# Optimization experiments

Measured on AMD Instinct MI355X. Metric: run time of the kernel, lower is better.

Reference implementation:

```python
import jax, jax.numpy as jnp
import numpy as np

TOKEN_SELF_ATTN_VALUE = -5e4  # reformer_pytorch constant for masking self-attention
BUCKET_SIZE = 64
N_HASHES = 4
HEADS = 8


def look_one_back(x):
    # concat each chunk with the previous chunk along the within-chunk axis (axis=2)
    prev = jnp.concatenate([x[:, -1:], x[:, :-1]], axis=1)
    return jnp.concatenate([prev, x], axis=2)


def lsh_attention(qk, v, rotations):
    # qk, v: (b*h, t, dh); rotations: (dh, n_hashes, n_buckets//2)
    bh, seqlen, dim = qk.shape
    n_buckets = seqlen // BUCKET_SIZE
    # --- LSH bucket hashing via random rotations ---
    rotated = jnp.einsum('btf,fhi->bhti', qk, rotations)            # (bh, H, t, nb/2)
    rotated = jnp.concatenate([rotated, -rotated], axis=-1)          # (bh, H, t, nb)
    buckets = jnp.argmax(rotated, axis=-1)                           # (bh, H, t)
    offsets = (jnp.arange(N_HASHES) * n_buckets)[None, :, None]
    buckets = (buckets + offsets).reshape(bh, N_HASHES * seqlen)
    # --- stable sort tokens by (bucket, position) ---
    ticker = jnp.arange(N_HASHES * seqlen)
    buckets_and_t = seqlen * buckets + (ticker % seqlen)[None, :]
    sticker = jnp.argsort(buckets_and_t, axis=-1)                    # sorted ticker
    undo_sort = jnp.argsort(sticker, axis=-1)
    st = sticker % seqlen                                            # original positions
    sqk = jnp.take_along_axis(qk, st[..., None], axis=1)
    sv = jnp.take_along_axis(v, st[..., None], axis=1)
    # --- chunk into n_hashes*n_buckets chunks of bucket_size tokens ---
    n_chunks = N_HASHES * n_buckets
    bq_t = st.reshape(bh, n_chunks, -1)
    bqk = sqk.reshape(bh, n_chunks, -1, dim)
    bv = sv.reshape(bh, n_chunks, -1, dim)
    bq = bqk
    bk = bqk / jnp.maximum(jnp.linalg.norm(bqk, axis=-1, keepdims=True), 1e-12)
    bk = look_one_back(bk)
    bv = look_one_back(bv)
    bkv_t = look_one_back(bq_t)
    # --- chunked attention with one-chunk lookback ---
    dots = jnp.einsum('bcie,bcje->bcij', bq, bk) * (dim ** -0.5)     # (bh, nc, bs, 2*bs)
    dots = jnp.where(bq_t[:, :, :, None] == bkv_t[:, :, None, :], TOKEN_SELF_ATTN_VALUE, dots)
    dots_lse = jax.nn.logsumexp(dots, axis=-1, keepdims=True)
    probs = jnp.exp(dots - dots_lse)
    bo = jnp.einsum('bcij,bcje->bcie', probs, bv)
    so = bo.reshape(bh, N_HASHES * seqlen, dim)
    slogits = dots_lse.reshape(bh, N_HASHES * seqlen)
    # --- unsort and combine hash rounds weighted by logsumexp ---
    o = jnp.take_along_axis(so, undo_sort[..., None], axis=1)
    logits = jnp.take_along_axis(slogits, undo_sort, axis=1)
    o = o.reshape(bh, N_HASHES, seqlen, dim)
    logits = logits.reshape(bh, N_HASHES, seqlen, 1)
    w = jnp.exp(logits - jax.nn.logsumexp(logits, axis=1, keepdims=True))
    return jnp.sum(o * w, axis=1)


def _forward(queries, Wqk, Wv, Wo, bo, rotations):
    B, N, C = queries.shape
    m = BUCKET_SIZE * 2
    if N % m != 0:  # fit_length: zero-pad to multiple of bucket_size*2 (static)
        pad = m - N % m
        x = jnp.concatenate([queries, jnp.zeros((B, pad, C), queries.dtype)], axis=1)
    else:
        x = queries
    T = x.shape[1]
    dh = C // HEADS
    qk = jnp.einsum('btc,cf->btf', x, Wqk).reshape(B, T, HEADS, dh).transpose(0, 2, 1, 3).reshape(B * HEADS, T, dh)
    v = jnp.einsum('btc,cf->btf', x, Wv).reshape(B, T, HEADS, dh).transpose(0, 2, 1, 3).reshape(B * HEADS, T, dh)
    out = lsh_attention(qk, v, rotations)
    out = out.reshape(B, HEADS, T, dh).transpose(0, 2, 1, 3).reshape(B, T, C)
    out = jnp.einsum('btc,cf->btf', out, Wo) + bo
    return out[:, :N]


def setup_inputs() -> dict:
    key = jax.random.key(0)
    ks = jax.random.split(key, 7)
    B, N, C = 4, 4096, 512
    dh = C // HEADS
    n_buckets = N // BUCKET_SIZE  # 64
    return {
        'queries': jax.random.normal(ks[0], (B, N, C), jnp.float32),
        'keys': jax.random.normal(ks[1], (B, N, C), jnp.float32),
        'values': jax.random.normal(ks[2], (B, N, C), jnp.float32),
        'attn_mask': jnp.zeros((1,), jnp.bool_),
        'tau': 1,
        'delta': 1,
        'Wqk': jax.random.normal(ks[3], (C, C), jnp.float32) / np.float32(np.sqrt(C)),
        'Wv': jax.random.normal(ks[4], (C, C), jnp.float32) / np.float32(np.sqrt(C)),
        'Wo': jax.random.normal(ks[5], (C, C), jnp.float32) / np.float32(np.sqrt(C)),
        'bo': jnp.zeros((C,), jnp.float32),
        'rotations': jax.random.normal(ks[6], (dh, N_HASHES, n_buckets // 2), jnp.float32),
    }


def reference(queries, keys, values, attn_mask, tau, delta, Wqk, Wv, Wo, bo, rotations):
    # keys/values/attn_mask/tau/delta are accepted but unused, matching the torch module
    return _forward(queries, Wqk, Wv, Wo, bo, rotations)
```

## Files before the change

kernel.cpp:

```cpp
#include <hip/hip_runtime.h>
#include <hip/hip_bf16.h>
#include <cstdint>
#include <cstddef>

#define LSEQ   4096
#define DHD    64
#define NHASH  4
#define CDIM   512
#define NBH    32
#define MROWS  16384
#define NCHUNK 256

typedef __attribute__((ext_vector_type(8))) short short8;
typedef __attribute__((ext_vector_type(4))) float f32x4;
typedef __attribute__((ext_vector_type(2))) float f32x2;

__device__ inline uint32_t f2bf(float f) {
  uint32_t u = __float_as_uint(f);
  return (u + 0x7FFFu + ((u >> 16) & 1u)) >> 16;
}
__device__ inline float bf2f(uint32_t h) { return __uint_as_float(h << 16); }
__device__ inline void split2(float f, uint32_t& hi, uint32_t& lo) {
  hi = f2bf(f);
  lo = f2bf(f - bf2f(hi));
}
__device__ inline short8 ldsK(const uint16_t* p) {
  union { uint2 u[2]; short8 s; } t;
  t.u[0] = *reinterpret_cast<const uint2*>(p);
  t.u[1] = *reinterpret_cast<const uint2*>(p + 4);
  return t.s;
}

__global__ __launch_bounds__(256) void prep_x_kernel(
    const float* __restrict__ X, uint16_t* __restrict__ X0,
    uint16_t* __restrict__ X1)
{
  size_t i = ((size_t)blockIdx.x * 256 + threadIdx.x) * 4;
  float4 v = *reinterpret_cast<const float4*>(X + i);
  uint32_t h[4], l[4];
#pragma unroll
  for (int j = 0; j < 4; j++) split2((&v.x)[j], h[j], l[j]);
  uint2 hw = {(h[1] << 16) | h[0], (h[3] << 16) | h[2]};
  uint2 lw = {(l[1] << 16) | l[0], (l[3] << 16) | l[2]};
  *reinterpret_cast<uint2*>(X0 + i) = hw;
  *reinterpret_cast<uint2*>(X1 + i) = lw;
}

__global__ __launch_bounds__(256) void prep_wv_kernel(
    const float* __restrict__ Wv,
    uint16_t* __restrict__ v0, uint16_t* __restrict__ v1)
{
  __shared__ float Ts[32][33];
  const int tid = threadIdx.x;
  const int k0 = blockIdx.x * 32, n0 = blockIdx.y * 32;
#pragma unroll
  for (int i = 0; i < 4; i++) {
    int flat = i * 256 + tid;
    int r = flat >> 5, c = flat & 31;
    Ts[r][c] = Wv[(size_t)(k0 + r) * 512 + n0 + c];
  }
  __syncthreads();
#pragma unroll
  for (int i = 0; i < 4; i++) {
    int flat = i * 256 + tid;
    int nr = flat >> 5, kc = flat & 31;
    uint32_t h, l;
    split2(Ts[kc][nr], h, l);
    size_t idx = (size_t)(n0 + nr) * 512 + k0 + kc;
    v0[idx] = (uint16_t)h;
    v1[idx] = (uint16_t)l;
  }
}

__global__ __launch_bounds__(256) void gemm_qk_kernel(
    const float* __restrict__ X, const float* __restrict__ Wqk,
    float* __restrict__ qk, uint16_t* __restrict__ qkhi,
    uint16_t* __restrict__ qklo, float* __restrict__ invn_g)
{
  const float* W = Wqk;
  const int m0 = blockIdx.x * 128;
  const int n0 = blockIdx.y * 64;
  __shared__ float As[32][132];
  __shared__ float Bs[32][68];
  const int tid = threadIdx.x;
  const int r = tid >> 4, c = tid & 15;
  f32x2 acc2[8][2];
#pragma unroll
  for (int i = 0; i < 8; i++) {
    acc2[i][0] = {0.f, 0.f};
    acc2[i][1] = {0.f, 0.f};
  }

  const int arow = tid >> 3;
  const int ac4  = tid & 7;
  const int brow = tid >> 4;
  const int bc4  = tid & 15;

  for (int kb = 0; kb < CDIM; kb += 32) {
#pragma unroll
    for (int rr = 0; rr < 4; rr++) {
      int m = arow + rr * 32;
      float4 av = *reinterpret_cast<const float4*>(&X[(size_t)(m0 + m) * CDIM + kb + ac4 * 4]);
      As[ac4 * 4 + 0][m] = av.x;
      As[ac4 * 4 + 1][m] = av.y;
      As[ac4 * 4 + 2][m] = av.z;
      As[ac4 * 4 + 3][m] = av.w;
    }
#pragma unroll
    for (int rr = 0; rr < 2; rr++) {
      int kk = brow + rr * 16;
      *reinterpret_cast<float4*>(&Bs[kk][bc4 * 4]) =
          *reinterpret_cast<const float4*>(&W[(size_t)(kb + kk) * CDIM + n0 + bc4 * 4]);
    }
    __syncthreads();
#pragma unroll
    for (int k = 0; k < 32; k++) {
      float4 a0 = *reinterpret_cast<const float4*>(&As[k][r * 8]);
      float4 a1 = *reinterpret_cast<const float4*>(&As[k][r * 8 + 4]);
      float4 b  = *reinterpret_cast<const float4*>(&Bs[k][c * 4]);
      float am[8] = {a0.x, a0.y, a0.z, a0.w, a1.x, a1.y, a1.z, a1.w};
      f32x2 b01 = {b.x, b.y};
      f32x2 b23 = {b.z, b.w};
#pragma unroll
      for (int i = 0; i < 8; i++) {
        f32x2 av = {am[i], am[i]};
        acc2[i][0] += av * b01;
        acc2[i][1] += av * b23;
      }
    }
    __syncthreads();
  }
  const int head = n0 >> 6;
#pragma unroll
  for (int ii = 0; ii < 8; ii++) {
    int m = m0 + r * 8 + ii;
    int b = m >> 12, t = m & 4095;
    size_t base = ((size_t)(b * 8 + head) * LSEQ + t) * DHD;
    float4 ov = {acc2[ii][0][0], acc2[ii][0][1], acc2[ii][1][0], acc2[ii][1][1]};
    *reinterpret_cast<float4*>(&qk[base + c * 4]) = ov;
    uint32_t h0, l0, h1, l1, h2, l2, h3, l3;
    split2(ov.x, h0, l0); split2(ov.y, h1, l1);
    split2(ov.z, h2, l2); split2(ov.w, h3, l3);
    uint2 hw = {(h1 << 16) | h0, (h3 << 16) | h2};
    uint2 lw = {(l1 << 16) | l0, (l3 << 16) | l2};
    *reinterpret_cast<uint2*>(&qkhi[base + c * 4]) = hw;
    *reinterpret_cast<uint2*>(&qklo[base + c * 4]) = lw;
    float ss = ov.x * ov.x + ov.y * ov.y + ov.z * ov.z + ov.w * ov.w;
    ss += __shfl_xor(ss, 1, 64);
    ss += __shfl_xor(ss, 2, 64);
    ss += __shfl_xor(ss, 4, 64);
    ss += __shfl_xor(ss, 8, 64);
    if (c == 0)
      invn_g[(size_t)(b * 8 + head) * LSEQ + t] = 1.0f / fmaxf(sqrtf(ss), 1e-12f);
  }
}

__global__ __launch_bounds__(512) void gemm_v_mfma_kernel(
    const uint16_t* __restrict__ X0g, const uint16_t* __restrict__ X1g,
    const uint16_t* __restrict__ Wv0, const uint16_t* __restrict__ Wv1,
    uint16_t* __restrict__ vhi)
{
  __shared__ __align__(16) uint16_t Xs[2 * 128 * 40];
  __shared__ __align__(16) uint16_t Ws[2 * 128 * 40];
  const int tid = threadIdx.x;
  const int m0 = blockIdx.x * 128;
  const int n0 = blockIdx.y * 128;
  const int lane = tid & 63, w = tid >> 6;
  const int l16 = lane & 15, lg = lane >> 4;

  f32x4 acc[8];
#pragma unroll
  for (int nt = 0; nt < 8; nt++) acc[nt] = {0.f, 0.f, 0.f, 0.f};

  const int srow = tid >> 3;
  const int sch = (tid & 7) * 4;

  for (int kb = 0; kb < CDIM; kb += 32) {
#pragma unroll
    for (int i = 0; i < 4; i++) {
      int p = i >> 1;
      int row = (i & 1) * 64 + srow;
      const uint16_t* xg = (p == 0) ? X0g : X1g;
      const uint16_t* wg = (p == 0) ? Wv0 : Wv1;
      *reinterpret_cast<uint2*>(Xs + p * 5120 + row * 40 + sch) =
          *reinterpret_cast<const uint2*>(xg + (size_t)(m0 + row) * 512 + kb + sch);
      *reinterpret_cast<uint2*>(Ws + p * 5120 + row * 40 + sch) =
          *reinterpret_cast<const uint2*>(wg + (size_t)(n0 + row) * 512 + kb + sch);
    }
    __syncthreads();

    const int abase = (w * 16 + l16) * 40 + lg * 8;
    short8 a0 = *reinterpret_cast<const short8*>(Xs + abase);
    short8 a1 = *reinterpret_cast<const short8*>(Xs + 5120 + abase);
#pragma unroll
    for (int nt = 0; nt < 8; nt++) {
      int bbase = (nt * 16 + l16) * 40 + lg * 8;
      short8 b0 = *reinterpret_cast<const short8*>(Ws + bbase);
      short8 b1 = *reinterpret_cast<const short8*>(Ws + 5120 + bbase);
      acc[nt] = __builtin_amdgcn_mfma_f32_16x16x32_bf16(a0, b0, acc[nt], 0, 0, 0);
      acc[nt] = __builtin_amdgcn_mfma_f32_16x16x32_bf16(a1, b0, acc[nt], 0, 0, 0);
      acc[nt] = __builtin_amdgcn_mfma_f32_16x16x32_bf16(a0, b1, acc[nt], 0, 0, 0);
    }
    __syncthreads();
  }

#pragma unroll
  for (int rr = 0; rr < 4; rr++) {
    int mg = m0 + w * 16 + lg * 4 + rr;
    int b = mg >> 12, t = mg & 4095;
#pragma unroll
    for (int nt = 0; nt < 8; nt++) {
      int head = (n0 >> 6) + (nt >> 2);
      size_t base = ((size_t)(b * 8 + head) * LSEQ + t) * DHD + (nt & 3) * 16 + l16;
      vhi[base] = (uint16_t)f2bf(acc[nt][rr]);
    }
  }
}

__global__ __launch_bounds__(256) void hash_kernel(
    const float* __restrict__ qk, const float* __restrict__ rot,
    int* __restrict__ buckets)
{
  __shared__ float rotT[128][68];
  const int tid = threadIdx.x;
  for (int idx = tid; idx < 64 * 128; idx += 256) {
    int f = idx >> 7, hi = idx & 127;
    rotT[hi][f] = rot[idx];
  }
  __syncthreads();
  const int bh = blockIdx.y;
  const int t = blockIdx.x * 256 + tid;
  float4 row4[16];
  const float* src = &qk[((size_t)bh * LSEQ + t) * DHD];
#pragma unroll
  for (int i = 0; i < 16; i++) row4[i] = reinterpret_cast<const float4*>(src)[i];

  int* bout = &buckets[(size_t)bh * NHASH * LSEQ];
  for (int h = 0; h < NHASH; h++) {
    float rc[32];
    float best = -3.0e38f;
    int bidx = 0;
#pragma unroll 4
    for (int i = 0; i < 32; i++) {
      const float* rr = &rotT[h * 32 + i][0];
      float a = 0.f;
#pragma unroll
      for (int f4 = 0; f4 < 16; f4++) {
        float4 rv = reinterpret_cast<const float4*>(rr)[f4];
        a += row4[f4].x * rv.x + row4[f4].y * rv.y + row4[f4].z * rv.z + row4[f4].w * rv.w;
      }
      rc[i] = a;
      if (a > best) { best = a; bidx = i; }
    }
#pragma unroll
    for (int i = 0; i < 32; i++) {
      float nv = -rc[i];
      if (nv > best) { best = nv; bidx = 32 + i; }
    }
    bout[h * LSEQ + t] = bidx;
  }
}

__global__ __launch_bounds__(256) void sort_kernel(
    const int* __restrict__ buckets, int* __restrict__ st)
{
  __shared__ int hist[64][64];
  const int h = blockIdx.x, bh = blockIdx.y;
  const int tid = threadIdx.x;
  const int* bk = &buckets[((size_t)bh * NHASH + h) * LSEQ];

  for (int i = tid; i < 64 * 64; i += 256) (&hist[0][0])[i] = 0;
  __syncthreads();
  for (int t = tid; t < LSEQ; t += 256) {
    int b = bk[t];
    atomicAdd(&hist[t >> 6][b], 1);
  }
  __syncthreads();
  if (tid < 64) {
    int tot = 0;
    for (int s = 0; s < 64; s++) tot += hist[s][tid];
    int vsc = tot;
    for (int off = 1; off < 64; off <<= 1) {
      int nv = __shfl_up(vsc, off, 64);
      if (tid >= off) vsc += nv;
    }
    int run = h * LSEQ + (vsc - tot);
    for (int s = 0; s < 64; s++) {
      int tmp = hist[s][tid];
      hist[s][tid] = run;
      run += tmp;
    }
  }
  __syncthreads();
  const int wave = tid >> 6, lane = tid & 63;
  for (int si = 0; si < 16; si++) {
    int seg = wave * 16 + si;
    int pos = seg * 64 + lane;
    int b = bk[pos];
    int rank = 0;
    for (int k = 0; k < 64; k++) {
      int bb = __shfl(b, k, 64);
      rank += (bb == b && k < lane) ? 1 : 0;
    }
    int dest = hist[seg][b] + rank;
    st[(size_t)bh * (NHASH * LSEQ) + dest] = pos;
  }
}

__global__ __launch_bounds__(256) void attn_kernel(
    const uint16_t* __restrict__ qkhi, const uint16_t* __restrict__ qklo,
    const uint16_t* __restrict__ vhi, const float* __restrict__ invn_g,
    const int* __restrict__ st, uint16_t* __restrict__ o,
    float* __restrict__ lse_out)
{
  __shared__ __align__(16) uint8_t smem[53248];
  uint16_t* Khi  = (uint16_t*)smem;
  uint16_t* Klo  = Khi + 128 * 68;
  uint16_t* Vthi = (uint16_t*)(smem + 34816);
  float*    invn = (float*)(smem + 52224);
  int*      kpos = (int*)(smem + 52736);
  uint32_t* P32  = (uint32_t*)smem;

  const int cchunk = blockIdx.x, bh = blockIdx.y;
  const int tid = threadIdx.x;
  const int prev = (cchunk + NCHUNK - 1) & (NCHUNK - 1);
  const int* stb = &st[(size_t)bh * (NHASH * LSEQ)];
  const int h = cchunk >> 6;

  if (tid < 128) {
    int kp = (tid < 64) ? stb[prev * 64 + tid] : stb[cchunk * 64 + (tid - 64)];
    kpos[tid] = kp;
    invn[tid] = invn_g[(size_t)bh * LSEQ + kp];
  }
  __syncthreads();

  {
    const int d4 = tid & 15, rbase = tid >> 4;
    const uint16_t* qhb = qkhi + (size_t)bh * LSEQ * DHD;
    const uint16_t* qlb = qklo + (size_t)bh * LSEQ * DHD;
#pragma unroll
    for (int it = 0; it < 8; it++) {
      int row = rbase + it * 16;
      size_t src = (size_t)kpos[row] * DHD + d4 * 4;
      *reinterpret_cast<uint2*>(Khi + row * 68 + d4 * 4) =
          *reinterpret_cast<const uint2*>(qhb + src);
      *reinterpret_cast<uint2*>(Klo + row * 68 + d4 * 4) =
          *reinterpret_cast<const uint2*>(qlb + src);
    }
  }
  {
    const int d4 = tid & 15, jg0 = tid >> 4;
    const uint16_t* vb = vhi + (size_t)bh * LSEQ * DHD;
#pragma unroll
    for (int half = 0; half < 2; half++) {
      int jg = jg0 + half * 16;
      uint2 vr[4];
#pragma unroll
      for (int s = 0; s < 4; s++)
        vr[s] = *reinterpret_cast<const uint2*>(vb + (size_t)kpos[jg * 4 + s] * DHD + d4 * 4);
#pragma unroll
      for (int i = 0; i < 4; i++) {
        int d = d4 * 4 + i;
        uint32_t e0 = (((i & 2) ? vr[0].y : vr[0].x) >> ((i & 1) * 16)) & 0xffffu;
        uint32_t e1 = (((i & 2) ? vr[1].y : vr[1].x) >> ((i & 1) * 16)) & 0xffffu;
        uint32_t e2 = (((i & 2) ? vr[2].y : vr[2].x) >> ((i & 1) * 16)) & 0xffffu;
        uint32_t e3 = (((i & 2) ? vr[3].y : vr[3].x) >> ((i & 1) * 16)) & 0xffffu;
        uint2 outw = {e0 | (e1 << 16), e2 | (e3 << 16)};
        int cpr = (jg >> 1) ^ (d & 15);
        *reinterpret_cast<uint2*>(Vthi + d * 128 + cpr * 8 + (jg & 1) * 4) = outw;
      }
    }
  }
  __syncthreads();

  const int lane = tid & 63, w = tid >> 6;
  const int l16 = lane & 15, lg = lane >> 4;

  f32x4 acc[8];
#pragma unroll
  for (int nt = 0; nt < 8; nt++) acc[nt] = {0.f, 0.f, 0.f, 0.f};

#pragma unroll
  for (int ks = 0; ks < 2; ks++) {
    int aoff = (64 + w * 16 + l16) * 68 + ks * 32 + lg * 8;
    short8 a_hi = ldsK(Khi + aoff);
    short8 a_lo = ldsK(Klo + aoff);
#pragma unroll
    for (int nt = 0; nt < 8; nt++) {
      int boff = (nt * 16 + l16) * 68 + ks * 32 + lg * 8;
      short8 b_hi = ldsK(Khi + boff);
      short8 b_lo = ldsK(Klo + boff);
      acc[nt] = __builtin_amdgcn_mfma_f32_16x16x32_bf16(a_hi, b_hi, acc[nt], 0, 0, 0);
      acc[nt] = __builtin_amdgcn_mfma_f32_16x16x32_bf16(a_lo, b_hi, acc[nt], 0, 0, 0);
      acc[nt] = __builtin_amdgcn_mfma_f32_16x16x32_bf16(a_hi, b_lo, acc[nt], 0, 0, 0);
    }
  }

  float invc[8]; int kpc[8];
#pragma unroll
  for (int nt = 0; nt < 8; nt++) {
    invc[nt] = invn[nt * 16 + l16] * 0.125f;
    kpc[nt] = kpos[nt * 16 + l16];
  }
  float pll[4];
#pragma unroll
  for (int r = 0; r < 4; r++) {
    int q = w * 16 + lg * 4 + r;
    int qp = kpos[64 + q];
    float mm = -3.0e38f;
#pragma unroll
    for (int nt = 0; nt < 8; nt++) {
      float s = acc[nt][r] * invc[nt];
      if (qp == kpc[nt]) s = -5e4f;
      acc[nt][r] = s;
      mm = fmaxf(mm, s);
    }
    mm = fmaxf(mm, __shfl_xor(mm, 1, 64));
    mm = fmaxf(mm, __shfl_xor(mm, 2, 64));
    mm = fmaxf(mm, __shfl_xor(mm, 4, 64));
    mm = fmaxf(mm, __shfl_xor(mm, 8, 64));
    float ll = 0.f;
#pragma unroll
    for (int nt = 0; nt < 8; nt++) {
      float p = __expf(acc[nt][r] - mm);
      acc[nt][r] = p;
      ll += p;
    }
    ll += __shfl_xor(ll, 1, 64);
    ll += __shfl_xor(ll, 2, 64);
    ll += __shfl_xor(ll, 4, 64);
    ll += __shfl_xor(ll, 8, 64);
    if (l16 == 0)
      lse_out[(size_t)bh * (NHASH * LSEQ) + h * LSEQ + qp] = mm + __logf(ll);
    pll[r] = 1.0f / ll;
  }
  __syncthreads();

#pragma unroll
  for (int r = 0; r < 4; r++) {
    int q = w * 16 + lg * 4 + r;
#pragma unroll
    for (int nt = 0; nt < 8; nt++) {
      uint32_t phi, plo;
      split2(acc[nt][r], phi, plo);
      P32[q * 132 + nt * 16 + l16] = (plo << 16) | phi;
    }
  }

  f32x4 oacc[4];
#pragma unroll
  for (int nt = 0; nt < 4; nt++) oacc[nt] = {0.f, 0.f, 0.f, 0.f};

#pragma unroll
  for (int ks = 0; ks < 4; ks++) {
    const uint32_t* pr = P32 + (w * 16 + l16) * 132 + ks * 32 + lg * 8;
    uint4 ua = *reinterpret_cast<const uint4*>(pr);
    uint4 ub = *reinterpret_cast<const uint4*>(pr + 4);
    uint32_t u[8] = {ua.x, ua.y, ua.z, ua.w, ub.x, ub.y, ub.z, ub.w};
    union { uint32_t w4[4]; short8 s8; } ph, pl;
#pragma unroll
    for (int k2 = 0; k2 < 4; k2++) {
      ph.w4[k2] = (u[2 * k2] & 0xffffu) | (u[2 * k2 + 1] << 16);
      pl.w4[k2] = (u[2 * k2] >> 16) | (u[2 * k2 + 1] & 0xffff0000u);
    }
    const int cc = ks * 4 + lg;
#pragma unroll
    for (int nt = 0; nt < 4; nt++) {
      int voff = (nt * 16 + l16) * 128 + ((cc ^ l16) & 15) * 8;
      short8 v_hi = *reinterpret_cast<const short8*>(Vthi + voff);
      oacc[nt] = __builtin_amdgcn_mfma_f32_16x16x32_bf16(ph.s8, v_hi, oacc[nt], 0, 0, 0);
      oacc[nt] = __builtin_amdgcn_mfma_f32_16x16x32_bf16(pl.s8, v_hi, oacc[nt], 0, 0, 0);
    }
  }

  {
    uint16_t* ob = o + ((size_t)bh * (NHASH * LSEQ) + (size_t)h * LSEQ) * DHD;
#pragma unroll
    for (int r = 0; r < 4; r++) {
      int q = w * 16 + lg * 4 + r;
      int qp = kpos[64 + q];
      float s = pll[r];
#pragma unroll
      for (int nt = 0; nt < 4; nt++)
        ob[(size_t)qp * DHD + nt * 16 + l16] = (uint16_t)f2bf(oacc[nt][r] * s);
    }
  }
}

__global__ __launch_bounds__(256) void combine_kernel(
    const uint16_t* __restrict__ o, const float* __restrict__ lse,
    uint16_t* __restrict__ comb_hi, uint16_t* __restrict__ comb_lo)
{
  int gid = blockIdx.x * 4 + (threadIdx.x >> 6);
  int lane = threadIdx.x & 63;
  int bh = gid >> 12;
  int pos = gid & 4095;
  const float* lb = &lse[(size_t)bh * (NHASH * LSEQ) + pos];
  float l0 = lb[0], l1 = lb[LSEQ], l2 = lb[2 * LSEQ], l3 = lb[3 * LSEQ];
  float m = fmaxf(fmaxf(l0, l1), fmaxf(l2, l3));
  float w0 = __expf(l0 - m), w1 = __expf(l1 - m), w2 = __expf(l2 - m), w3 = __expf(l3 - m);
  float inv = 1.0f / (w0 + w1 + w2 + w3);
  const uint16_t* ob = &o[((size_t)bh * (NHASH * LSEQ) + pos) * DHD];
  float val = (w0 * bf2f(ob[lane]) + w1 * bf2f(ob[(size_t)LSEQ * DHD + lane]) +
               w2 * bf2f(ob[(size_t)2 * LSEQ * DHD + lane]) +
               w3 * bf2f(ob[(size_t)3 * LSEQ * DHD + lane])) * inv;
  int b = bh >> 3, head = bh & 7;
  size_t idx = ((size_t)(b * LSEQ + pos)) * CDIM + head * DHD + lane;
  uint32_t hi, lo;
  split2(val, hi, lo);
  comb_hi[idx] = (uint16_t)hi;
  comb_lo[idx] = (uint16_t)lo;
}

__global__ __launch_bounds__(256) void prep_wo_kernel(
    const float* __restrict__ Wo, uint16_t* __restrict__ th,
    uint16_t* __restrict__ tl)
{
  int idx = blockIdx.x * 256 + threadIdx.x;
  int k = idx >> 9, n = idx & 511;
  uint32_t hi, lo;
  split2(Wo[idx], hi, lo);
  th[n * 512 + k] = (uint16_t)hi;
  tl[n * 512 + k] = (uint16_t)lo;
}

__global__ __launch_bounds__(256) void gemm_out_kernel(
    const uint16_t* __restrict__ Ahi_g, const uint16_t* __restrict__ Alo_g,
    const uint16_t* __restrict__ Bhi_g, const uint16_t* __restrict__ Blo_g,
    const float* __restrict__ bias, float* __restrict__ out)
{
  __shared__ __align__(16) uint16_t Ah[128 * 40];
  __shared__ __align__(16) uint16_t Al[128 * 40];
  __shared__ __align__(16) uint16_t Bh[128 * 40];
  __shared__ __align__(16) uint16_t Bl[128 * 40];
  const int tid = threadIdx.x;
  const int m0 = blockIdx.x * 128, n0 = blockIdx.y * 128;
  const int lane = tid & 63, w = tid >> 6;
  const int l16 = lane & 15, lg = lane >> 4;
  const int mq = w >> 1, nq = w & 1;
  f32x4 acc[4][4];
#pragma unroll
  for (int i = 0; i < 4; i++)
#pragma unroll
    for (int j = 0; j < 4; j++) acc[i][j] = {0.f, 0.f, 0.f, 0.f};

  const int srow = tid >> 1, sh = tid & 1;
  for (int kb = 0; kb < CDIM; kb += 32) {
    {
      const uint4* sa_h = (const uint4*)(Ahi_g + (size_t)(m0 + srow) * CDIM + kb + sh * 16);
      const uint4* sa_l = (const uint4*)(Alo_g + (size_t)(m0 + srow) * CDIM + kb + sh * 16);
      const uint4* sb_h = (const uint4*)(Bhi_g + (size_t)(n0 + srow) * CDIM + kb + sh * 16);
      const uint4* sb_l = (const uint4*)(Blo_g + (size_t)(n0 + srow) * CDIM + kb + sh * 16);
      uint4* da_h = (uint4*)(Ah + srow * 40 + sh * 16);
      uint4* da_l = (uint4*)(Al + srow * 40 + sh * 16);
      uint4* db_h = (uint4*)(Bh + srow * 40 + sh * 16);
      uint4* db_l = (uint4*)(Bl + srow * 40 + sh * 16);
      da_h[0] = sa_h[0]; da_h[1] = sa_h[1];
      da_l[0] = sa_l[0]; da_l[1] = sa_l[1];
      db_h[0] = sb_h[0]; db_h[1] = sb_h[1];
      db_l[0] = sb_l[0]; db_l[1] = sb_l[1];
    }
    __syncthreads();
    short8 fa_h[4], fa_l[4], fb_h[4], fb_l[4];
#pragma unroll
    for (int mt = 0; mt < 4; mt++) {
      int ao = (mq * 64 + mt * 16 + l16) * 40 + lg * 8;
      fa_h[mt] = *reinterpret_cast<const short8*>(Ah + ao);
      fa_l[mt] = *reinterpret_cast<const short8*>(Al + ao);
    }
#pragma unroll
    for (int nt = 0; nt < 4; nt++) {
      int bo_ = (nq * 64 + nt * 16 + l16) * 40 + lg * 8;
      fb_h[nt] = *reinterpret_cast<const short8*>(Bh + bo_);
      fb_l[nt] = *reinterpret_cast<const short8*>(Bl + bo_);
    }
#pragma unroll
    for (int mt = 0; mt < 4; mt++)
#pragma unroll
      for (int nt = 0; nt < 4; nt++) {
        acc[mt][nt] = __builtin_amdgcn_mfma_f32_16x16x32_bf16(fa_h[mt], fb_h[nt], acc[mt][nt], 0, 0, 0);
        acc[mt][nt] = __builtin_amdgcn_mfma_f32_16x16x32_bf16(fa_l[mt], fb_h[nt], acc[mt][nt], 0, 0, 0);
        acc[mt][nt] = __builtin_amdgcn_mfma_f32_16x16x32_bf16(fa_h[mt], fb_l[nt], acc[mt][nt], 0, 0, 0);
      }
    __syncthreads();
  }
#pragma unroll
  for (int nt = 0; nt < 4; nt++) {
    int n = n0 + nq * 64 + nt * 16 + l16;
    float bv = bias[n];
#pragma unroll
    for (int mt = 0; mt < 4; mt++) {
#pragma unroll
      for (int rr = 0; rr < 4; rr++) {
        int m = m0 + mq * 64 + mt * 16 + lg * 4 + rr;
        out[(size_t)m * CDIM + n] = acc[mt][nt][rr] + bv;
      }
    }
  }
}

extern "C" void kernel_launch(void* const* d_in, const int* in_sizes, int n_in,
                              void* d_out, int out_size, void* d_ws, size_t ws_size,
                              hipStream_t stream) {
  (void)in_sizes; (void)n_in; (void)out_size; (void)ws_size;
  const float* X    = (const float*)d_in[0];
  const float* Wqk  = (const float*)d_in[6];
  const float* Wv   = (const float*)d_in[7];
  const float* Wo   = (const float*)d_in[8];
  const float* bo   = (const float*)d_in[9];
  const float* rot  = (const float*)d_in[10];

  uint8_t* W = (uint8_t*)d_ws;
  float*    qk      = (float*)(W + 0);
  uint16_t* obuf    = (uint16_t*)(W + 33554432);
  uint16_t* qkhi    = (uint16_t*)(W + 100663296);
  uint16_t* qklo    = (uint16_t*)(W + 117440512);
  uint16_t* vhi     = (uint16_t*)(W + 134217728);
  int*      buckets = (int*)(W + 150994944);
  int*      st      = (int*)(W + 153092096);
  float*    lse     = (float*)(W + 155189248);
  float*    invn_g  = (float*)(W + 157286400);
  uint16_t* woT_hi  = (uint16_t*)(W + 157810688);
  uint16_t* woT_lo  = (uint16_t*)(W + 158334976);
  uint16_t* wvT0    = (uint16_t*)(W + 158859264);
  uint16_t* wvT1    = (uint16_t*)(W + 159383552);
  uint16_t* x0      = (uint16_t*)(W + 33554432);
  uint16_t* x1      = (uint16_t*)(W + 50331648);
  uint16_t* comb_hi = (uint16_t*)(W + 0);
  uint16_t* comb_lo = (uint16_t*)(W + 16777216);

  hipLaunchKernelGGL(prep_x_kernel, dim3(8192), dim3(256), 0, stream,
                     X, x0, x1);
  hipLaunchKernelGGL(prep_wv_kernel, dim3(16, 16), dim3(256), 0, stream,
                     Wv, wvT0, wvT1);
  hipLaunchKernelGGL(gemm_qk_kernel, dim3(128, 8), dim3(256), 0, stream,
                     X, Wqk, qk, qkhi, qklo, invn_g);
  hipLaunchKernelGGL(gemm_v_mfma_kernel, dim3(128, 4), dim3(512), 0, stream,
                     x0, x1, wvT0, wvT1, vhi);
  hipLaunchKernelGGL(hash_kernel, dim3(16, 32), dim3(256), 0, stream,
                     qk, rot, buckets);
  hipLaunchKernelGGL(sort_kernel, dim3(4, 32), dim3(256), 0, stream,
                     buckets, st);
  hipLaunchKernelGGL(prep_wo_kernel, dim3(1024), dim3(256), 0, stream,
                     Wo, woT_hi, woT_lo);
  hipLaunchKernelGGL(attn_kernel, dim3(256, 32), dim3(256), 0, stream,
                     qkhi, qklo, vhi, invn_g, st, obuf, lse);
  hipLaunchKernelGGL(combine_kernel, dim3(32768), dim3(256), 0, stream,
                     obuf, lse, comb_hi, comb_lo);
  hipLaunchKernelGGL(gemm_out_kernel, dim3(128, 4), dim3(256), 0, stream,
                     comb_hi, comb_lo, woT_hi, woT_lo, bo, (float*)d_out);
}
```

Baseline: 460.1 us.

## Merge prep kernels, widen QK GEMM tile, use packed bf16 converts, remap attention blocks

Folds the three weight/input preparation kernels into one launch, which removes two kernel launches. The fp32 QK GEMM tile is widened to 128 columns so each thread computes 8x8 outputs. Software bf16 rounding is replaced with the hardware v_cvt_pk_bf16_f32 instruction across several kernels. Attention blocks are remapped so each XCD handles a contiguous group of heads, aiming for better L2 locality. The wider tile raises register pressure and halves the QK grid, which can reduce occupancy.

```diff
diff --git a/kernel.cpp b/kernel.cpp
--- a/kernel.cpp
+++ b/kernel.cpp
@@ -24,6 +24,11 @@
   hi = f2bf(f);
   lo = f2bf(f - bf2f(hi));
 }
+__device__ inline uint32_t cvtpk_bf16(float a, float b) {
+  uint32_t r;
+  asm("v_cvt_pk_bf16_f32 %0, %1, %2" : "=v"(r) : "v"(a), "v"(b));
+  return r;
+}
 __device__ inline short8 ldsK(const uint16_t* p) {
   union { uint2 u[2]; short8 s; } t;
   t.u[0] = *reinterpret_cast<const uint2*>(p);
@@ -31,44 +36,55 @@
   return t.s;
 }
 
-__global__ __launch_bounds__(256) void prep_x_kernel(
-    const float* __restrict__ X, uint16_t* __restrict__ X0,
-    uint16_t* __restrict__ X1)
-{
-  size_t i = ((size_t)blockIdx.x * 256 + threadIdx.x) * 4;
-  float4 v = *reinterpret_cast<const float4*>(X + i);
-  uint32_t h[4], l[4];
-#pragma unroll
-  for (int j = 0; j < 4; j++) split2((&v.x)[j], h[j], l[j]);
-  uint2 hw = {(h[1] << 16) | h[0], (h[3] << 16) | h[2]};
-  uint2 lw = {(l[1] << 16) | l[0], (l[3] << 16) | l[2]};
-  *reinterpret_cast<uint2*>(X0 + i) = hw;
-  *reinterpret_cast<uint2*>(X1 + i) = lw;
-}
-
-__global__ __launch_bounds__(256) void prep_wv_kernel(
-    const float* __restrict__ Wv,
-    uint16_t* __restrict__ v0, uint16_t* __restrict__ v1)
+__global__ __launch_bounds__(256) void prep_kernel(
+    const float* __restrict__ X, const float* __restrict__ Wv,
+    const float* __restrict__ Wo,
+    uint16_t* __restrict__ X0, uint16_t* __restrict__ X1,
+    uint16_t* __restrict__ wvT0, uint16_t* __restrict__ wvT1,
+    uint16_t* __restrict__ woT_hi, uint16_t* __restrict__ woT_lo)
 {
   __shared__ float Ts[32][33];
-  const int tid = threadIdx.x;
-  const int k0 = blockIdx.x * 32, n0 = blockIdx.y * 32;
-#pragma unroll
-  for (int i = 0; i < 4; i++) {
-    int flat = i * 256 + tid;
-    int r = flat >> 5, c = flat & 31;
-    Ts[r][c] = Wv[(size_t)(k0 + r) * 512 + n0 + c];
-  }
-  __syncthreads();
-#pragma unroll
-  for (int i = 0; i < 4; i++) {
-    int flat = i * 256 + tid;
-    int nr = flat >> 5, kc = flat & 31;
-    uint32_t h, l;
-    split2(Ts[kc][nr], h, l);
-    size_t idx = (size_t)(n0 + nr) * 512 + k0 + kc;
-    v0[idx] = (uint16_t)h;
-    v1[idx] = (uint16_t)l;
+  const int bid = blockIdx.x, tid = threadIdx.x;
+  if (bid < 8192) {
+    size_t i = ((size_t)bid * 256 + tid) * 4;
+    float4 v = *reinterpret_cast<const float4*>(X + i);
+    uint32_t h01 = cvtpk_bf16(v.x, v.y);
+    uint32_t h23 = cvtpk_bf16(v.z, v.w);
+    float r0 = v.x - __uint_as_float(h01 << 16);
+    float r1 = v.y - __uint_as_float(h01 & 0xffff0000u);
+    float r2 = v.z - __uint_as_float(h23 << 16);
+    float r3 = v.w - __uint_as_float(h23 & 0xffff0000u);
+    uint2 hw = {h01, h23};
+    uint2 lw = {cvtpk_bf16(r0, r1), cvtpk_bf16(r2, r3)};
+    *reinterpret_cast<uint2*>(X0 + i) = hw;
+    *reinterpret_cast<uint2*>(X1 + i) = lw;
+  } else if (bid < 9216) {
+    int idx = (bid - 8192) * 256 + tid;
+    int k = idx >> 9, n = idx & 511;
+    uint32_t hi, lo;
+    split2(Wo[idx], hi, lo);
+    woT_hi[n * 512 + k] = (uint16_t)hi;
+    woT_lo[n * 512 + k] = (uint16_t)lo;
+  } else {
+    int wb = bid - 9216;
+    const int k0 = (wb >> 4) * 32, n0 = (wb & 15) * 32;
+#pragma unroll
+    for (int i = 0; i < 4; i++) {
+      int flat = i * 256 + tid;
+      int r = flat >> 5, c = flat & 31;
+      Ts[r][c] = Wv[(size_t)(k0 + r) * 512 + n0 + c];
+    }
+    __syncthreads();
+#pragma unroll
+    for (int i = 0; i < 4; i++) {
+      int flat = i * 256 + tid;
+      int nr = flat >> 5, kc = flat & 31;
+      uint32_t h, l;
+      split2(Ts[kc][nr], h, l);
+      size_t idx = (size_t)(n0 + nr) * 512 + k0 + kc;
+      wvT0[idx] = (uint16_t)h;
+      wvT1[idx] = (uint16_t)l;
+    }
   }
 }
 
@@ -77,24 +93,22 @@
     float* __restrict__ qk, uint16_t* __restrict__ qkhi,
     uint16_t* __restrict__ qklo, float* __restrict__ invn_g)
 {
-  const float* W = Wqk;
   const int m0 = blockIdx.x * 128;
-  const int n0 = blockIdx.y * 64;
+  const int n0 = blockIdx.y * 128;
   __shared__ float As[32][132];
-  __shared__ float Bs[32][68];
+  __shared__ float Bs[32][132];
   const int tid = threadIdx.x;
   const int r = tid >> 4, c = tid & 15;
-  f32x2 acc2[8][2];
-#pragma unroll
-  for (int i = 0; i < 8; i++) {
-    acc2[i][0] = {0.f, 0.f};
-    acc2[i][1] = {0.f, 0.f};
-  }
+  f32x2 acc2[8][4];
+#pragma unroll
+  for (int i = 0; i < 8; i++)
+#pragma unroll
+    for (int j = 0; j < 4; j++) acc2[i][j] = {0.f, 0.f};
 
   const int arow = tid >> 3;
   const int ac4  = tid & 7;
-  const int brow = tid >> 4;
-  const int bc4  = tid & 15;
+  const int brow = tid >> 5;
+  const int bc4  = tid & 31;
 
   for (int kb = 0; kb < CDIM; kb += 32) {
 #pragma unroll
@@ -107,50 +121,61 @@
       As[ac4 * 4 + 3][m] = av.w;
     }
 #pragma unroll
-    for (int rr = 0; rr < 2; rr++) {
-      int kk = brow + rr * 16;
+    for (int rr = 0; rr < 4; rr++) {
+      int kk = brow + rr * 8;
       *reinterpret_cast<float4*>(&Bs[kk][bc4 * 4]) =
-          *reinterpret_cast<const float4*>(&W[(size_t)(kb + kk) * CDIM + n0 + bc4 * 4]);
+          *reinterpret_cast<const float4*>(&Wqk[(size_t)(kb + kk) * CDIM + n0 + bc4 * 4]);
     }
     __syncthreads();
 #pragma unroll
     for (int k = 0; k < 32; k++) {
       float4 a0 = *reinterpret_cast<const float4*>(&As[k][r * 8]);
       float4 a1 = *reinterpret_cast<const float4*>(&As[k][r * 8 + 4]);
-      float4 b  = *reinterpret_cast<const float4*>(&Bs[k][c * 4]);
+      float4 b0 = *reinterpret_cast<const float4*>(&Bs[k][c * 8]);
+      float4 b1 = *reinterpret_cast<const float4*>(&Bs[k][c * 8 + 4]);
       float am[8] = {a0.x, a0.y, a0.z, a0.w, a1.x, a1.y, a1.z, a1.w};
-      f32x2 b01 = {b.x, b.y};
-      f32x2 b23 = {b.z, b.w};
+      f32x2 bp[4] = {{b0.x, b0.y}, {b0.z, b0.w}, {b1.x, b1.y}, {b1.z, b1.w}};
 #pragma unroll
       for (int i = 0; i < 8; i++) {
         f32x2 av = {am[i], am[i]};
-        acc2[i][0] += av * b01;
-        acc2[i][1] += av * b23;
+#pragma unroll
+        for (int jp = 0; jp < 4; jp++)
+          acc2[i][jp] += av * bp[jp];
       }
     }
     __syncthreads();
   }
-  const int head = n0 >> 6;
+  const int head = (n0 >> 6) + (c >> 3);
 #pragma unroll
   for (int ii = 0; ii < 8; ii++) {
     int m = m0 + r * 8 + ii;
     int b = m >> 12, t = m & 4095;
-    size_t base = ((size_t)(b * 8 + head) * LSEQ + t) * DHD;
-    float4 ov = {acc2[ii][0][0], acc2[ii][0][1], acc2[ii][1][0], acc2[ii][1][1]};
-    *reinterpret_cast<float4*>(&qk[base + c * 4]) = ov;
-    uint32_t h0, l0, h1, l1, h2, l2, h3, l3;
-    split2(ov.x, h0, l0); split2(ov.y, h1, l1);
-    split2(ov.z, h2, l2); split2(ov.w, h3, l3);
-    uint2 hw = {(h1 << 16) | h0, (h3 << 16) | h2};
-    uint2 lw = {(l1 << 16) | l0, (l3 << 16) | l2};
-    *reinterpret_cast<uint2*>(&qkhi[base + c * 4]) = hw;
-    *reinterpret_cast<uint2*>(&qklo[base + c * 4]) = lw;
-    float ss = ov.x * ov.x + ov.y * ov.y + ov.z * ov.z + ov.w * ov.w;
+    size_t base = ((size_t)(b * 8 + head) * LSEQ + t) * DHD + (c & 7) * 8;
+    float vals[8] = {acc2[ii][0][0], acc2[ii][0][1], acc2[ii][1][0], acc2[ii][1][1],
+                     acc2[ii][2][0], acc2[ii][2][1], acc2[ii][3][0], acc2[ii][3][1]};
+    *reinterpret_cast<float4*>(&qk[base]) = {vals[0], vals[1], vals[2], vals[3]};
+    *reinterpret_cast<float4*>(&qk[base + 4]) = {vals[4], vals[5], vals[6], vals[7]};
+    uint32_t hw[4], lw[4];
+#pragma unroll
+    for (int p = 0; p < 4; p++) {
+      float x = vals[2 * p], y = vals[2 * p + 1];
+      uint32_t h = cvtpk_bf16(x, y);
+      float rx = x - __uint_as_float(h << 16);
+      float ry = y - __uint_as_float(h & 0xffff0000u);
+      hw[p] = h;
+      lw[p] = cvtpk_bf16(rx, ry);
+    }
+    *reinterpret_cast<uint2*>(&qkhi[base]) = {hw[0], hw[1]};
+    *reinterpret_cast<uint2*>(&qkhi[base + 4]) = {hw[2], hw[3]};
+    *reinterpret_cast<uint2*>(&qklo[base]) = {lw[0], lw[1]};
+    *reinterpret_cast<uint2*>(&qklo[base + 4]) = {lw[2], lw[3]};
+    float ss = 0.f;
+#pragma unroll
+    for (int j = 0; j < 8; j++) ss += vals[j] * vals[j];
     ss += __shfl_xor(ss, 1, 64);
     ss += __shfl_xor(ss, 2, 64);
     ss += __shfl_xor(ss, 4, 64);
-    ss += __shfl_xor(ss, 8, 64);
-    if (c == 0)
+    if ((c & 7) == 0)
       invn_g[(size_t)(b * 8 + head) * LSEQ + t] = 1.0f / fmaxf(sqrtf(ss), 1e-12f);
   }
 }
@@ -212,7 +237,7 @@
     for (int nt = 0; nt < 8; nt++) {
       int head = (n0 >> 6) + (nt >> 2);
       size_t base = ((size_t)(b * 8 + head) * LSEQ + t) * DHD + (nt & 3) * 16 + l16;
-      vhi[base] = (uint16_t)f2bf(acc[nt][rr]);
+      vhi[base] = (uint16_t)cvtpk_bf16(acc[nt][rr], acc[nt][rr]);
     }
   }
 }
@@ -321,7 +346,11 @@
   int*      kpos = (int*)(smem + 52736);
   uint32_t* P32  = (uint32_t*)smem;
 
-  const int cchunk = blockIdx.x, bh = blockIdx.y;
+  const int lin = blockIdx.y * 256 + blockIdx.x;
+  const int xcd = lin & 7, sidx = lin >> 3;
+  const int bh = (xcd << 2) | (sidx >> 8);
+  const int cchunk = sidx & 255;
+
   const int tid = threadIdx.x;
   const int prev = (cchunk + NCHUNK - 1) & (NCHUNK - 1);
   const int* stb = &st[(size_t)bh * (NHASH * LSEQ)];
@@ -441,9 +470,10 @@
     int q = w * 16 + lg * 4 + r;
 #pragma unroll
     for (int nt = 0; nt < 8; nt++) {
-      uint32_t phi, plo;
-      split2(acc[nt][r], phi, plo);
-      P32[q * 132 + nt * 16 + l16] = (plo << 16) | phi;
+      float p = acc[nt][r];
+      uint32_t t1 = cvtpk_bf16(p, p);
+      float res = p - __uint_as_float(t1 << 16);
+      P32[q * 132 + nt * 16 + l16] = cvtpk_bf16(p, res);
     }
   }
 
@@ -481,8 +511,10 @@
       int qp = kpos[64 + q];
       float s = pll[r];
 #pragma unroll
-      for (int nt = 0; nt < 4; nt++)
-        ob[(size_t)qp * DHD + nt * 16 + l16] = (uint16_t)f2bf(oacc[nt][r] * s);
+      for (int nt = 0; nt < 4; nt++) {
+        float v = oacc[nt][r] * s;
+        ob[(size_t)qp * DHD + nt * 16 + l16] = (uint16_t)cvtpk_bf16(v, v);
+      }
     }
   }
 }
@@ -506,22 +538,10 @@
                w3 * bf2f(ob[(size_t)3 * LSEQ * DHD + lane])) * inv;
   int b = bh >> 3, head = bh & 7;
   size_t idx = ((size_t)(b * LSEQ + pos)) * CDIM + head * DHD + lane;
-  uint32_t hi, lo;
-  split2(val, hi, lo);
-  comb_hi[idx] = (uint16_t)hi;
-  comb_lo[idx] = (uint16_t)lo;
-}
-
-__global__ __launch_bounds__(256) void prep_wo_kernel(
-    const float* __restrict__ Wo, uint16_t* __restrict__ th,
-    uint16_t* __restrict__ tl)
-{
-  int idx = blockIdx.x * 256 + threadIdx.x;
-  int k = idx >> 9, n = idx & 511;
-  uint32_t hi, lo;
-  split2(Wo[idx], hi, lo);
-  th[n * 512 + k] = (uint16_t)hi;
-  tl[n * 512 + k] = (uint16_t)lo;
+  uint32_t hw = cvtpk_bf16(val, val);
+  float res = val - __uint_as_float(hw << 16);
+  comb_hi[idx] = (uint16_t)hw;
+  comb_lo[idx] = (uint16_t)cvtpk_bf16(res, res);
 }
 
 __global__ __launch_bounds__(256) void gemm_out_kernel(
@@ -629,11 +649,9 @@
   uint16_t* comb_hi = (uint16_t*)(W + 0);
   uint16_t* comb_lo = (uint16_t*)(W + 16777216);
 
-  hipLaunchKernelGGL(prep_x_kernel, dim3(8192), dim3(256), 0, stream,
-                     X, x0, x1);
-  hipLaunchKernelGGL(prep_wv_kernel, dim3(16, 16), dim3(256), 0, stream,
-                     Wv, wvT0, wvT1);
-  hipLaunchKernelGGL(gemm_qk_kernel, dim3(128, 8), dim3(256), 0, stream,
+  hipLaunchKernelGGL(prep_kernel, dim3(9472), dim3(256), 0, stream,
+                     X, Wv, Wo, x0, x1, wvT0, wvT1, woT_hi, woT_lo);
+  hipLaunchKernelGGL(gemm_qk_kernel, dim3(128, 4), dim3(256), 0, stream,
                      X, Wqk, qk, qkhi, qklo, invn_g);
   hipLaunchKernelGGL(gemm_v_mfma_kernel, dim3(128, 4), dim3(512), 0, stream,
                      x0, x1, wvT0, wvT1, vhi);
@@ -641,8 +659,6 @@
                      qk, rot, buckets);
   hipLaunchKernelGGL(sort_kernel, dim3(4, 32), dim3(256), 0, stream,
                      buckets, st);
-  hipLaunchKernelGGL(prep_wo_kernel, dim3(1024), dim3(256), 0, stream,
-                     Wo, woT_hi, woT_lo);
   hipLaunchKernelGGL(attn_kernel, dim3(256, 32), dim3(256), 0, stream,
                      qkhi, qklo, vhi, invn_g, st, obuf, lse);
   hipLaunchKernelGGL(combine_kernel, dim3(32768), dim3(256), 0, stream,
```

Measured after the change: 439.6 us. -4.5%, faster.
